# Kernel tuning notes

Measured on AMD Instinct MI355X. Metric: run time of the kernel, lower is better.

## Reference

```python
import jax, jax.numpy as jnp
import numpy as np

NUM_HEAD = 8
EPS = 1e-12  # matches torch F.normalize default eps


def setup_inputs() -> dict:
    key = jax.random.key(0)
    k1, k2, k3 = jax.random.split(key, 3)
    B, N, C = 8, 8192, 384
    x = jax.random.normal(k1, (B, N, C), dtype=jnp.float32)
    # torch Linear weights: (out_features, in_features)
    w_qkv = jax.random.normal(k2, (3 * C, C), dtype=jnp.float32) * (C ** -0.5)
    w_proj = jax.random.normal(k3, (C, C), dtype=jnp.float32) * (C ** -0.5)
    b_proj = jnp.zeros((C,), dtype=jnp.float32)
    return {"x": x, "w_qkv": w_qkv, "w_proj": w_proj, "b_proj": b_proj}


def _l2norm(t):
    # F.normalize(t, dim=-1): t / max(||t||_2, eps)
    n = jnp.sqrt(jnp.sum(t * t, axis=-1, keepdims=True))
    return t / jnp.maximum(n, EPS)


def reference(x, w_qkv, w_proj, b_proj):
    B, N, C = x.shape
    H = NUM_HEAD
    Dh = C // H
    qkv = x @ w_qkv.T  # (B, N, 3C), qkv_bias=False
    qkv = qkv.reshape(B, N, 3, H, Dh).transpose(2, 0, 3, 1, 4)  # (3, B, H, N, Dh)
    q, k, v = qkv[0], qkv[1], qkv[2]
    # transpose(-2, -1) -> (B, H, Dh, N); normalize along N (cross-covariance attn)
    q = _l2norm(jnp.swapaxes(q, -2, -1))
    k = _l2norm(jnp.swapaxes(k, -2, -1))
    v = jnp.swapaxes(v, -2, -1)  # (B, H, Dh, N)
    attn = jnp.einsum('bhdn,bhen->bhde', q, k)  # (B, H, Dh, Dh)
    attn = jax.nn.softmax(attn, axis=-1)
    out = jnp.einsum('bhde,bhen->bhdn', attn, v)  # (B, H, Dh, N)
    out = out.transpose(0, 3, 1, 2).reshape(B, N, C)  # (B, N, C)
    out = out @ w_proj.T + b_proj
    return out
```

## Files before the change

kernel.cpp:

```cpp
#include <hip/hip_runtime.h>
#include <hip/hip_bf16.h>
#include <stdint.h>


typedef __bf16 bf16_t;
typedef __attribute__((ext_vector_type(8))) __bf16 bf16x8;
typedef __attribute__((ext_vector_type(4))) __bf16 bf16x4;
typedef __attribute__((ext_vector_type(4))) float f32x4;

#define NTOK 8192
#define CDIM 384
#define WH   25165824
#define DHN  393216

#define XCHUNKS 3145728
#define TCHUNKS 3201024

__device__ __forceinline__ f32x4 mfma16(bf16x8 a, bf16x8 b, f32x4 c) {
  return __builtin_amdgcn_mfma_f32_16x16x32_bf16(a, b, c, 0, 0, 0);
}

__device__ __forceinline__ void gload16(bf16_t* lds, const bf16_t* g) {
  __builtin_amdgcn_global_load_lds(
      (const __attribute__((address_space(1))) void*)g,
      (__attribute__((address_space(3))) void*)lds, 16, 0, 0);
}

template <bool BF16>
__device__ __forceinline__ bf16x8 load8(const void* p, int idx) {
  if constexpr (BF16) {
    return *(const bf16x8*)((const bf16_t*)p + idx);
  } else {
    const float* f = (const float*)p + idx;
    f32x4 a = *(const f32x4*)f;
    f32x4 b = *(const f32x4*)(f + 4);
    bf16x8 r;
    r[0] = (bf16_t)a[0]; r[1] = (bf16_t)a[1]; r[2] = (bf16_t)a[2]; r[3] = (bf16_t)a[3];
    r[4] = (bf16_t)b[0]; r[5] = (bf16_t)b[1]; r[6] = (bf16_t)b[2]; r[7] = (bf16_t)b[3];
    return r;
  }
}

__global__ void k_probe(const uint32_t* __restrict__ X, int* __restrict__ flag) {
  __shared__ int cnt;
  if (threadIdx.x == 0) cnt = 0;
  __syncthreads();
  const uint32_t w = X[threadIdx.x];
  const int e = (int)((w >> 7) & 0xFF);
  const int sane = (e >= 110 && e <= 131) ? 1 : 0;
  atomicAdd(&cnt, sane);
  __syncthreads();
  if (threadIdx.x == 0) *flag = (cnt >= 128) ? 1 : 0;
}

__global__ void k_zero(float* __restrict__ p, int n) {
  int i = blockIdx.x * 256 + threadIdx.x;
  if (i < n) p[i] = 0.f;
}

__global__ void k_cvt(const void* __restrict__ X, const void* __restrict__ Wqkv,
                      bf16_t* __restrict__ Xb, bf16_t* __restrict__ Wb,
                      const int* __restrict__ flagp) {
  const int isb = *flagp;
  const int G = gridDim.x * 256;
  for (int c = blockIdx.x * 256 + threadIdx.x; c < TCHUNKS; c += G) {
    const bool isX = c < XCHUNKS;
    const int lc = isX ? c : c - XCHUNKS;
    const void* src = isX ? X : Wqkv;
    bf16_t* dst = (isX ? Xb : Wb) + (size_t)lc * 8;
    if (isb) {
      *(bf16x8*)dst = *((const bf16x8*)src + lc);
    } else {
      const f32x4 a = *((const f32x4*)src + lc * 2);
      const f32x4 b = *((const f32x4*)src + lc * 2 + 1);
      bf16x8 r;
      r[0] = (bf16_t)a[0]; r[1] = (bf16_t)a[1]; r[2] = (bf16_t)a[2]; r[3] = (bf16_t)a[3];
      r[4] = (bf16_t)b[0]; r[5] = (bf16_t)b[1]; r[6] = (bf16_t)b[2]; r[7] = (bf16_t)b[3];
      *(bf16x8*)dst = r;
    }
  }
}

template <bool BF16, bool GL>
__device__ __forceinline__ void qkv_body(const void* __restrict__ X,
                                         const void* __restrict__ Wqkv,
                                         bf16_t* __restrict__ qkv,
                                         bf16_t* As, bf16_t* Bs) {
  const int tid = threadIdx.x;
  const int lane = tid & 63;
  const int wr = tid >> 7, wc = (tid >> 6) & 1;
  const int q4 = lane >> 4, l16 = lane & 15;
  const int rowB0 = blockIdx.x * 128;
  const int r0 = tid >> 2, kk = (tid & 3) << 3;
  const int bb = rowB0 >> 13;
  const int nB = rowB0 & 8191;

  const bf16_t* XB = (const bf16_t*)X;
  const bf16_t* WB = (const bf16_t*)Wqkv;

  for (int jt = 0; jt < 9; jt++) {
    const int rowA0 = jt * 128;
    const int which = jt / 3;
    const int jtt = jt - which * 3;
    f32x4 acc[4][4];
#pragma unroll
    for (int i = 0; i < 4; i++)
#pragma unroll
      for (int j = 0; j < 4; j++) acc[i][j] = (f32x4){0.f, 0.f, 0.f, 0.f};

    for (int k0 = 0; k0 < CDIM; k0 += 32) {
      if constexpr (GL) {
        __syncthreads();
        gload16(As + tid * 8,         WB + (rowA0 + r0) * CDIM + k0 + kk);
        gload16(As + (tid + 256) * 8, WB + (rowA0 + r0 + 64) * CDIM + k0 + kk);
        gload16(Bs + tid * 8,         XB + (rowB0 + r0) * CDIM + k0 + kk);
        gload16(Bs + (tid + 256) * 8, XB + (rowB0 + r0 + 64) * CDIM + k0 + kk);
        __syncthreads();
      } else {
        bf16x8 a0 = load8<BF16>(Wqkv, (rowA0 + r0) * CDIM + k0 + kk);
        bf16x8 a1 = load8<BF16>(Wqkv, (rowA0 + r0 + 64) * CDIM + k0 + kk);
        bf16x8 b0 = load8<BF16>(X, (rowB0 + r0) * CDIM + k0 + kk);
        bf16x8 b1 = load8<BF16>(X, (rowB0 + r0 + 64) * CDIM + k0 + kk);
        __syncthreads();
        *(bf16x8*)&As[tid * 8] = a0;
        *(bf16x8*)&As[(tid + 256) * 8] = a1;
        *(bf16x8*)&Bs[tid * 8] = b0;
        *(bf16x8*)&Bs[(tid + 256) * 8] = b1;
        __syncthreads();
      }
      bf16x8 af[4], bfr[4];
#pragma unroll
      for (int i = 0; i < 4; i++) {
        af[i]  = *(const bf16x8*)&As[(wr * 64 + i * 16 + l16) * 32 + q4 * 8];
        bfr[i] = *(const bf16x8*)&Bs[(wc * 64 + i * 16 + l16) * 32 + q4 * 8];
      }
      if (which < 2) {
#pragma unroll
        for (int i = 0; i < 4; i++)
#pragma unroll
          for (int j = 0; j < 4; j++) acc[i][j] = mfma16(bfr[j], af[i], acc[i][j]);
      } else {
#pragma unroll
        for (int i = 0; i < 4; i++)
#pragma unroll
          for (int j = 0; j < 4; j++) acc[i][j] = mfma16(af[i], bfr[j], acc[i][j]);
      }
    }

    if (which < 2) {
#pragma unroll
      for (int i = 0; i < 4; i++) {
        const int rin = jtt * 128 + wr * 64 + i * 16 + l16;
        const int h = rin / 48, dh = rin - h * 48;
        bf16_t* rowp = qkv + which * WH + (bb * 8 + h) * DHN + dh * NTOK
                       + nB + wc * 64 + q4 * 4;
#pragma unroll
        for (int j = 0; j < 4; j++) {
          bf16x4 o = {(bf16_t)acc[i][j][0], (bf16_t)acc[i][j][1],
                      (bf16_t)acc[i][j][2], (bf16_t)acc[i][j][3]};
          *(bf16x4*)(rowp + j * 16) = o;
        }
      }
    } else {
#pragma unroll
      for (int i = 0; i < 4; i++) {
        const int rin0 = jtt * 128 + wr * 64 + i * 16 + q4 * 4;
#pragma unroll
        for (int j = 0; j < 4; j++) {
          const int mg = rowB0 + wc * 64 + j * 16 + l16;
          bf16x4 o = {(bf16_t)acc[i][j][0], (bf16_t)acc[i][j][1],
                      (bf16_t)acc[i][j][2], (bf16_t)acc[i][j][3]};
          *(bf16x4*)(qkv + 2 * WH + mg * CDIM + rin0) = o;
        }
      }
    }
  }
}

__global__ __launch_bounds__(256, 2) void k_gemm_qkv(
    const bf16_t* __restrict__ Xb, const bf16_t* __restrict__ Wb,
    bf16_t* __restrict__ qkv) {
  __shared__ __align__(16) bf16_t As[128 * 32];
  __shared__ __align__(16) bf16_t Bs[128 * 32];
  qkv_body<true, true>(Xb, Wb, qkv, As, Bs);
}

__global__ __launch_bounds__(256, 2) void k_gemm_qkv_bf16(
    const void* __restrict__ X, const void* __restrict__ Wqkv,
    bf16_t* __restrict__ qkv, const int* __restrict__ flagp) {
  __shared__ __align__(16) bf16_t As[128 * 32];
  __shared__ __align__(16) bf16_t Bs[128 * 32];
  if (!*flagp) return;
  qkv_body<true, false>(X, Wqkv, qkv, As, Bs);
}

__global__ __launch_bounds__(256, 2) void k_gemm_qkv_f32(
    const void* __restrict__ X, const void* __restrict__ Wqkv,
    bf16_t* __restrict__ qkv, const int* __restrict__ flagp) {
  __shared__ __align__(16) bf16_t As[128 * 32];
  __shared__ __align__(16) bf16_t Bs[128 * 32];
  if (*flagp) return;
  qkv_body<false, false>(X, Wqkv, qkv, As, Bs);
}

__global__ __launch_bounds__(256, 2) void k_gram(
    const bf16_t* __restrict__ qkv, float* __restrict__ S_acc, float* __restrict__ ssq_acc) {
  __shared__ __align__(16) float sm[9312];
  bf16_t* Qs = (bf16_t*)sm;
  bf16_t* Ks = Qs + 6144;
  float* ssq_sm = sm + 9216;

  const int tid = threadIdx.x;
  const int wave = tid >> 6, lane = tid & 63, q4 = lane >> 4, l16 = lane & 15;
  const int s = blockIdx.x, bh = blockIdx.y;
  const bf16_t* Qg = qkv + bh * DHN;
  const bf16_t* Kg = qkv + WH + bh * DHN;

  if (tid < 96) ssq_sm[tid] = 0.f;

  f32x4 acc[3][3];
#pragma unroll
  for (int i = 0; i < 3; i++)
#pragma unroll
    for (int j = 0; j < 3; j++) acc[i][j] = (f32x4){0.f, 0.f, 0.f, 0.f};
  float qss[3] = {0.f, 0.f, 0.f}, kss[3] = {0.f, 0.f, 0.f};

  for (int t0 = 0; t0 < 8; t0++) {
    const int n0 = s * 1024 + t0 * 128;
    bf16x8 qv[3], kv[3];
#pragma unroll
    for (int jj = 0; jj < 3; jj++) {
      const int c = jj * 256 + tid;
      const int st = c / 192, rem = c - st * 192;
      const int row = rem >> 2, kk = (rem & 3) << 3;
      const int gofs = row * NTOK + n0 + st * 32 + kk;
      qv[jj] = *(const bf16x8*)(Qg + gofs);
      kv[jj] = *(const bf16x8*)(Kg + gofs);
    }
    __syncthreads();
#pragma unroll
    for (int jj = 0; jj < 3; jj++) {
      *(bf16x8*)&Qs[(jj * 256 + tid) * 8] = qv[jj];
      *(bf16x8*)&Ks[(jj * 256 + tid) * 8] = kv[jj];
    }
    __syncthreads();
    bf16x8 qf[3], kf[3];
#pragma unroll
    for (int i = 0; i < 3; i++) {
      qf[i] = *(const bf16x8*)&Qs[wave * 1536 + (i * 16 + l16) * 32 + q4 * 8];
      kf[i] = *(const bf16x8*)&Ks[wave * 1536 + (i * 16 + l16) * 32 + q4 * 8];
    }
#pragma unroll
    for (int i = 0; i < 3; i++) {
#pragma unroll
      for (int u = 0; u < 8; u++) {
        const float qv2 = (float)qf[i][u], kv2 = (float)kf[i][u];
        qss[i] += qv2 * qv2;
        kss[i] += kv2 * kv2;
      }
#pragma unroll
      for (int j = 0; j < 3; j++) acc[i][j] = mfma16(qf[i], kf[j], acc[i][j]);
    }
  }

  __syncthreads();
  float* red = sm;
#pragma unroll
  for (int i = 0; i < 3; i++)
#pragma unroll
    for (int j = 0; j < 3; j++)
#pragma unroll
      for (int r = 0; r < 4; r++)
        red[wave * 2304 + (i * 3 + j) * 256 + lane * 4 + r] = acc[i][j][r];
#pragma unroll
  for (int i = 0; i < 3; i++) {
    atomicAdd(&ssq_sm[i * 16 + l16], qss[i]);
    atomicAdd(&ssq_sm[48 + i * 16 + l16], kss[i]);
  }
  __syncthreads();
  for (int idx = tid; idx < 2304; idx += 256) {
    const float v = red[idx] + red[2304 + idx] + red[4608 + idx] + red[6912 + idx];
    const int tile = idx >> 8, ln = (idx >> 2) & 63, r = idx & 3;
    const int i = tile / 3, j = tile - i * 3;
    const int d = i * 16 + ((ln >> 4) << 2) + r;
    const int e = j * 16 + (ln & 15);
    atomicAdd(&S_acc[bh * 2304 + d * 48 + e], v);
  }
  if (tid < 96) atomicAdd(&ssq_acc[bh * 96 + tid], ssq_sm[tid]);
}

__global__ void k_softmax(const float* __restrict__ S_acc, const float* __restrict__ ssq_acc,
                          float* __restrict__ attn_f) {
  __shared__ float invk_sm[48];
  const int bh = blockIdx.x, d = threadIdx.x;
  if (d < 48) invk_sm[d] = 1.f / fmaxf(sqrtf(ssq_acc[bh * 96 + 48 + d]), 1e-12f);
  __syncthreads();
  if (d < 48) {
    const float invq = 1.f / fmaxf(sqrtf(ssq_acc[bh * 96 + d]), 1e-12f);
    float lg[48], mx = -1e30f;
#pragma unroll
    for (int e = 0; e < 48; e++) {
      lg[e] = S_acc[bh * 2304 + d * 48 + e] * invq * invk_sm[e];
      mx = fmaxf(mx, lg[e]);
    }
    float ssum = 0.f;
#pragma unroll
    for (int e = 0; e < 48; e++) { lg[e] = expf(lg[e] - mx); ssum += lg[e]; }
    const float inv = 1.f / ssum;
#pragma unroll
    for (int e = 0; e < 48; e++) attn_f[bh * 2304 + d * 48 + e] = lg[e] * inv;
  }
}

__global__ void k_weff(
    const float* __restrict__ attn_f, const void* __restrict__ Wp,
    bf16_t* __restrict__ Weff, const int* __restrict__ flagp) {
  __shared__ float a_sm[2304];
  __shared__ float w_sm[2304];
  const int isb = *flagp;
  const int bid = blockIdx.x;
  const int ct = bid & 7, h = (bid >> 3) & 7, b = bid >> 6;
  const int bh = b * 8 + h;
  const int tid = threadIdx.x;

  for (int i = tid; i < 2304; i += 256) {
    a_sm[i] = attn_f[bh * 2304 + i];
    const int r = i / 48, c = i - r * 48;
    const int gi = (ct * 48 + r) * CDIM + h * 48 + c;
    w_sm[i] = isb ? (float)((const bf16_t*)Wp)[gi] : ((const float*)Wp)[gi];
  }
  __syncthreads();

  for (int o = tid; o < 2304; o += 256) {
    const int r = o / 48, e = o - r * 48;
    float s = 0.f;
#pragma unroll 8
    for (int d = 0; d < 48; d++) s += w_sm[r * 48 + d] * a_sm[d * 48 + e];
    Weff[b * 147456 + (ct * 48 + r) * CDIM + h * 48 + e] = (bf16_t)s;
  }
}

__global__ __launch_bounds__(256, 2) void k_gemm_out(
    const bf16_t* __restrict__ Weff, const bf16_t* __restrict__ qkv,
    const void* __restrict__ bias, void* __restrict__ out, const int* __restrict__ flagp) {
  __shared__ __align__(16) bf16_t As[128 * 32];
  __shared__ __align__(16) bf16_t Bs[128 * 32];
  const int isb = *flagp;
  const int tid = threadIdx.x;
  const int lane = tid & 63;
  const int wr = tid >> 7, wc = (tid >> 6) & 1;
  const int q4 = lane >> 4, l16 = lane & 15;
  const int b = blockIdx.y;
  const int rowB0 = blockIdx.x * 128;
  const bf16_t* Aa = Weff + b * 147456;
  const bf16_t* Ba = qkv + 2 * WH + b * (NTOK * CDIM);
  const int r0 = tid >> 2, kk = (tid & 3) << 3;

  for (int ct = 0; ct < 3; ct++) {
    const int rowA0 = ct * 128;
    f32x4 acc[4][4];
#pragma unroll
    for (int i = 0; i < 4; i++)
#pragma unroll
      for (int j = 0; j < 4; j++) acc[i][j] = (f32x4){0.f, 0.f, 0.f, 0.f};

    for (int k0 = 0; k0 < CDIM; k0 += 32) {
      __syncthreads();
      gload16(As + tid * 8,         Aa + (rowA0 + r0) * CDIM + k0 + kk);
      gload16(As + (tid + 256) * 8, Aa + (rowA0 + r0 + 64) * CDIM + k0 + kk);
      gload16(Bs + tid * 8,         Ba + (rowB0 + r0) * CDIM + k0 + kk);
      gload16(Bs + (tid + 256) * 8, Ba + (rowB0 + r0 + 64) * CDIM + k0 + kk);
      __syncthreads();
      bf16x8 af[4], bfr[4];
#pragma unroll
      for (int i = 0; i < 4; i++) {
        af[i]  = *(const bf16x8*)&As[(wr * 64 + i * 16 + l16) * 32 + q4 * 8];
        bfr[i] = *(const bf16x8*)&Bs[(wc * 64 + i * 16 + l16) * 32 + q4 * 8];
      }
#pragma unroll
      for (int i = 0; i < 4; i++)
#pragma unroll
        for (int j = 0; j < 4; j++) acc[i][j] = mfma16(af[i], bfr[j], acc[i][j]);
    }

#pragma unroll
    for (int i = 0; i < 4; i++) {
      const int cg = rowA0 + wr * 64 + i * 16 + q4 * 4;
      float bv[4];
#pragma unroll
      for (int r = 0; r < 4; r++)
        bv[r] = isb ? (float)((const bf16_t*)bias)[cg + r] : ((const float*)bias)[cg + r];
#pragma unroll
      for (int j = 0; j < 4; j++) {
        const int ng = rowB0 + wc * 64 + j * 16 + l16;
        const int oi = (b * NTOK + ng) * CDIM + cg;
        if (isb) {
          bf16x4 o = {(bf16_t)(acc[i][j][0] + bv[0]), (bf16_t)(acc[i][j][1] + bv[1]),
                      (bf16_t)(acc[i][j][2] + bv[2]), (bf16_t)(acc[i][j][3] + bv[3])};
          *(bf16x4*)((bf16_t*)out + oi) = o;
        } else {
          f32x4 o = {acc[i][j][0] + bv[0], acc[i][j][1] + bv[1],
                     acc[i][j][2] + bv[2], acc[i][j][3] + bv[3]};
          *(f32x4*)((float*)out + oi) = o;
        }
      }
    }
  }
}

extern "C" void kernel_launch(void* const* d_in, const int* in_sizes, int n_in,
                              void* d_out, int out_size, void* d_ws, size_t ws_size,
                              hipStream_t stream) {
  (void)in_sizes; (void)n_in; (void)out_size;
  const void* X    = d_in[0];
  const void* Wqkv = d_in[1];
  const void* Wp   = d_in[2];
  const void* bias = d_in[3];

  char* ws = (char*)d_ws;
  bf16_t* qkv    = (bf16_t*)ws;
  float*  S_acc  = (float*)(ws + 150994944);
  float*  ssq    = (float*)(ws + 151584768);
  float*  attn_f = (float*)(ws + 151609344);
  bf16_t* Weff   = (bf16_t*)(ws + 152199168);
  int*    flag   = (int*)(ws + 154558464);
  bf16_t* Xb     = (bf16_t*)(ws + 154558720);
  bf16_t* Wb     = (bf16_t*)(ws + 204890368);

  const bool have_cvt_ws = ws_size >= 205775104ULL;

  k_probe<<<dim3(1), 256, 0, stream>>>((const uint32_t*)X, flag);
  k_zero<<<dim3(600), 256, 0, stream>>>(S_acc, 153600);
  if (have_cvt_ws) {
    k_cvt<<<dim3(2048), 256, 0, stream>>>(X, Wqkv, Xb, Wb, flag);
    k_gemm_qkv<<<dim3(512), 256, 0, stream>>>(Xb, Wb, qkv);
  } else {
    k_gemm_qkv_bf16<<<dim3(512), 256, 0, stream>>>(X, Wqkv, qkv, flag);
    k_gemm_qkv_f32<<<dim3(512), 256, 0, stream>>>(X, Wqkv, qkv, flag);
  }
  k_gram<<<dim3(8, 64), 256, 0, stream>>>(qkv, S_acc, ssq);
  k_softmax<<<dim3(64), 64, 0, stream>>>(S_acc, ssq, attn_f);
  k_weff<<<dim3(512), 256, 0, stream>>>(attn_f, Wp, Weff, flag);
  k_gemm_out<<<dim3(64, 8), 256, 0, stream>>>(Weff, qkv, bias, d_out, flag);
}
```

Baseline: 407.1 us.

## Double-buffer LDS tiles in QKV and output GEMMs to overlap loads with MFMA

Adds ping-pong LDS buffers to the direct-to-LDS QKV GEMM and the output GEMM. The next k-slice (crossing output-tile boundaries) is issued before computing on the current one, with one barrier per iteration instead of two. This is meant to hide global load latency behind MFMA work, at the cost of doubling LDS use per block, which may reduce occupancy. The legacy register-staged paths are split into a separate function and left unchanged.

```diff
diff --git a/kernel.cpp b/kernel.cpp
--- a/kernel.cpp
+++ b/kernel.cpp
@@ -81,11 +81,10 @@
   }
 }
 
-template <bool BF16, bool GL>
-__device__ __forceinline__ void qkv_body(const void* __restrict__ X,
-                                         const void* __restrict__ Wqkv,
-                                         bf16_t* __restrict__ qkv,
-                                         bf16_t* As, bf16_t* Bs) {
+__device__ __forceinline__ void qkv_body_pipe(const bf16_t* __restrict__ XB,
+                                              const bf16_t* __restrict__ WB,
+                                              bf16_t* __restrict__ qkv,
+                                              bf16_t* As, bf16_t* Bs) {
   const int tid = threadIdx.x;
   const int lane = tid & 63;
   const int wr = tid >> 7, wc = (tid >> 6) & 1;
@@ -95,11 +94,22 @@
   const int bb = rowB0 >> 13;
   const int nB = rowB0 & 8191;
 
-  const bf16_t* XB = (const bf16_t*)X;
-  const bf16_t* WB = (const bf16_t*)Wqkv;
+  auto STAGE = [&](int jts, int ks, int nxt) {
+    const int rowA0 = jts * 128;
+    const int k0 = ks * 32;
+    bf16_t* Ad = As + nxt * 4096;
+    bf16_t* Bd = Bs + nxt * 4096;
+    gload16(Ad + tid * 8,         WB + (rowA0 + r0) * CDIM + k0 + kk);
+    gload16(Ad + (tid + 256) * 8, WB + (rowA0 + r0 + 64) * CDIM + k0 + kk);
+    gload16(Bd + tid * 8,         XB + (rowB0 + r0) * CDIM + k0 + kk);
+    gload16(Bd + (tid + 256) * 8, XB + (rowB0 + r0 + 64) * CDIM + k0 + kk);
+  };
+
+  STAGE(0, 0, 0);
+  __syncthreads();
+  int cur = 0;
 
   for (int jt = 0; jt < 9; jt++) {
-    const int rowA0 = jt * 128;
     const int which = jt / 3;
     const int jtt = jt - which * 3;
     f32x4 acc[4][4];
@@ -108,31 +118,19 @@
 #pragma unroll
       for (int j = 0; j < 4; j++) acc[i][j] = (f32x4){0.f, 0.f, 0.f, 0.f};
 
-    for (int k0 = 0; k0 < CDIM; k0 += 32) {
-      if constexpr (GL) {
-        __syncthreads();
-        gload16(As + tid * 8,         WB + (rowA0 + r0) * CDIM + k0 + kk);
-        gload16(As + (tid + 256) * 8, WB + (rowA0 + r0 + 64) * CDIM + k0 + kk);
-        gload16(Bs + tid * 8,         XB + (rowB0 + r0) * CDIM + k0 + kk);
-        gload16(Bs + (tid + 256) * 8, XB + (rowB0 + r0 + 64) * CDIM + k0 + kk);
-        __syncthreads();
-      } else {
-        bf16x8 a0 = load8<BF16>(Wqkv, (rowA0 + r0) * CDIM + k0 + kk);
-        bf16x8 a1 = load8<BF16>(Wqkv, (rowA0 + r0 + 64) * CDIM + k0 + kk);
-        bf16x8 b0 = load8<BF16>(X, (rowB0 + r0) * CDIM + k0 + kk);
-        bf16x8 b1 = load8<BF16>(X, (rowB0 + r0 + 64) * CDIM + k0 + kk);
-        __syncthreads();
-        *(bf16x8*)&As[tid * 8] = a0;
-        *(bf16x8*)&As[(tid + 256) * 8] = a1;
-        *(bf16x8*)&Bs[tid * 8] = b0;
-        *(bf16x8*)&Bs[(tid + 256) * 8] = b1;
-        __syncthreads();
-      }
+    for (int k = 0; k < 12; k++) {
+      if (!(jt == 8 && k == 11)) {
+        int kn = k + 1, jn = jt;
+        if (kn == 12) { kn = 0; jn = jt + 1; }
+        STAGE(jn, kn, cur ^ 1);
+      }
+      const bf16_t* Ac = As + cur * 4096;
+      const bf16_t* Bc = Bs + cur * 4096;
       bf16x8 af[4], bfr[4];
 #pragma unroll
       for (int i = 0; i < 4; i++) {
-        af[i]  = *(const bf16x8*)&As[(wr * 64 + i * 16 + l16) * 32 + q4 * 8];
-        bfr[i] = *(const bf16x8*)&Bs[(wc * 64 + i * 16 + l16) * 32 + q4 * 8];
+        af[i]  = *(const bf16x8*)&Ac[(wr * 64 + i * 16 + l16) * 32 + q4 * 8];
+        bfr[i] = *(const bf16x8*)&Bc[(wc * 64 + i * 16 + l16) * 32 + q4 * 8];
       }
       if (which < 2) {
 #pragma unroll
@@ -145,6 +143,8 @@
 #pragma unroll
           for (int j = 0; j < 4; j++) acc[i][j] = mfma16(af[i], bfr[j], acc[i][j]);
       }
+      __syncthreads();
+      cur ^= 1;
     }
 
     if (which < 2) {
@@ -180,9 +180,93 @@
 __global__ __launch_bounds__(256, 2) void k_gemm_qkv(
     const bf16_t* __restrict__ Xb, const bf16_t* __restrict__ Wb,
     bf16_t* __restrict__ qkv) {
-  __shared__ __align__(16) bf16_t As[128 * 32];
-  __shared__ __align__(16) bf16_t Bs[128 * 32];
-  qkv_body<true, true>(Xb, Wb, qkv, As, Bs);
+  __shared__ __align__(16) bf16_t As[2 * 4096];
+  __shared__ __align__(16) bf16_t Bs[2 * 4096];
+  qkv_body_pipe(Xb, Wb, qkv, As, Bs);
+}
+
+template <bool BF16>
+__device__ __forceinline__ void qkv_body_legacy(const void* __restrict__ X,
+                                                const void* __restrict__ Wqkv,
+                                                bf16_t* __restrict__ qkv,
+                                                bf16_t* As, bf16_t* Bs) {
+  const int tid = threadIdx.x;
+  const int lane = tid & 63;
+  const int wr = tid >> 7, wc = (tid >> 6) & 1;
+  const int q4 = lane >> 4, l16 = lane & 15;
+  const int rowB0 = blockIdx.x * 128;
+  const int r0 = tid >> 2, kk = (tid & 3) << 3;
+  const int bb = rowB0 >> 13;
+  const int nB = rowB0 & 8191;
+
+  for (int jt = 0; jt < 9; jt++) {
+    const int rowA0 = jt * 128;
+    const int which = jt / 3;
+    const int jtt = jt - which * 3;
+    f32x4 acc[4][4];
+#pragma unroll
+    for (int i = 0; i < 4; i++)
+#pragma unroll
+      for (int j = 0; j < 4; j++) acc[i][j] = (f32x4){0.f, 0.f, 0.f, 0.f};
+
+    for (int k0 = 0; k0 < CDIM; k0 += 32) {
+      bf16x8 a0 = load8<BF16>(Wqkv, (rowA0 + r0) * CDIM + k0 + kk);
+      bf16x8 a1 = load8<BF16>(Wqkv, (rowA0 + r0 + 64) * CDIM + k0 + kk);
+      bf16x8 b0 = load8<BF16>(X, (rowB0 + r0) * CDIM + k0 + kk);
+      bf16x8 b1 = load8<BF16>(X, (rowB0 + r0 + 64) * CDIM + k0 + kk);
+      __syncthreads();
+      *(bf16x8*)&As[tid * 8] = a0;
+      *(bf16x8*)&As[(tid + 256) * 8] = a1;
+      *(bf16x8*)&Bs[tid * 8] = b0;
+      *(bf16x8*)&Bs[(tid + 256) * 8] = b1;
+      __syncthreads();
+      bf16x8 af[4], bfr[4];
+#pragma unroll
+      for (int i = 0; i < 4; i++) {
+        af[i]  = *(const bf16x8*)&As[(wr * 64 + i * 16 + l16) * 32 + q4 * 8];
+        bfr[i] = *(const bf16x8*)&Bs[(wc * 64 + i * 16 + l16) * 32 + q4 * 8];
+      }
+      if (which < 2) {
+#pragma unroll
+        for (int i = 0; i < 4; i++)
+#pragma unroll
+          for (int j = 0; j < 4; j++) acc[i][j] = mfma16(bfr[j], af[i], acc[i][j]);
+      } else {
+#pragma unroll
+        for (int i = 0; i < 4; i++)
+#pragma unroll
+          for (int j = 0; j < 4; j++) acc[i][j] = mfma16(af[i], bfr[j], acc[i][j]);
+      }
+    }
+
+    if (which < 2) {
+#pragma unroll
+      for (int i = 0; i < 4; i++) {
+        const int rin = jtt * 128 + wr * 64 + i * 16 + l16;
+        const int h = rin / 48, dh = rin - h * 48;
+        bf16_t* rowp = qkv + which * WH + (bb * 8 + h) * DHN + dh * NTOK
+                       + nB + wc * 64 + q4 * 4;
+#pragma unroll
+        for (int j = 0; j < 4; j++) {
+          bf16x4 o = {(bf16_t)acc[i][j][0], (bf16_t)acc[i][j][1],
+                      (bf16_t)acc[i][j][2], (bf16_t)acc[i][j][3]};
+          *(bf16x4*)(rowp + j * 16) = o;
+        }
+      }
+    } else {
+#pragma unroll
+      for (int i = 0; i < 4; i++) {
+        const int rin0 = jtt * 128 + wr * 64 + i * 16 + q4 * 4;
+#pragma unroll
+        for (int j = 0; j < 4; j++) {
+          const int mg = rowB0 + wc * 64 + j * 16 + l16;
+          bf16x4 o = {(bf16_t)acc[i][j][0], (bf16_t)acc[i][j][1],
+                      (bf16_t)acc[i][j][2], (bf16_t)acc[i][j][3]};
+          *(bf16x4*)(qkv + 2 * WH + mg * CDIM + rin0) = o;
+        }
+      }
+    }
+  }
 }
 
 __global__ __launch_bounds__(256, 2) void k_gemm_qkv_bf16(
@@ -191,7 +275,7 @@
   __shared__ __align__(16) bf16_t As[128 * 32];
   __shared__ __align__(16) bf16_t Bs[128 * 32];
   if (!*flagp) return;
-  qkv_body<true, false>(X, Wqkv, qkv, As, Bs);
+  qkv_body_legacy<true>(X, Wqkv, qkv, As, Bs);
 }
 
 __global__ __launch_bounds__(256, 2) void k_gemm_qkv_f32(
@@ -200,7 +284,7 @@
   __shared__ __align__(16) bf16_t As[128 * 32];
   __shared__ __align__(16) bf16_t Bs[128 * 32];
   if (*flagp) return;
-  qkv_body<false, false>(X, Wqkv, qkv, As, Bs);
+  qkv_body_legacy<false>(X, Wqkv, qkv, As, Bs);
 }
 
 __global__ __launch_bounds__(256, 2) void k_gram(
@@ -343,8 +427,8 @@
 __global__ __launch_bounds__(256, 2) void k_gemm_out(
     const bf16_t* __restrict__ Weff, const bf16_t* __restrict__ qkv,
     const void* __restrict__ bias, void* __restrict__ out, const int* __restrict__ flagp) {
-  __shared__ __align__(16) bf16_t As[128 * 32];
-  __shared__ __align__(16) bf16_t Bs[128 * 32];
+  __shared__ __align__(16) bf16_t As[2 * 4096];
+  __shared__ __align__(16) bf16_t Bs[2 * 4096];
   const int isb = *flagp;
   const int tid = threadIdx.x;
   const int lane = tid & 63;
@@ -356,6 +440,21 @@
   const bf16_t* Ba = qkv + 2 * WH + b * (NTOK * CDIM);
   const int r0 = tid >> 2, kk = (tid & 3) << 3;
 
+  auto STAGE = [&](int cts, int ks, int nxt) {
+    const int rowA0 = cts * 128;
+    const int k0 = ks * 32;
+    bf16_t* Ad = As + nxt * 4096;
+    bf16_t* Bd = Bs + nxt * 4096;
+    gload16(Ad + tid * 8,         Aa + (rowA0 + r0) * CDIM + k0 + kk);
+    gload16(Ad + (tid + 256) * 8, Aa + (rowA0 + r0 + 64) * CDIM + k0 + kk);
+    gload16(Bd + tid * 8,         Ba + (rowB0 + r0) * CDIM + k0 + kk);
+    gload16(Bd + (tid + 256) * 8, Ba + (rowB0 + r0 + 64) * CDIM + k0 + kk);
+  };
+
+  STAGE(0, 0, 0);
+  __syncthreads();
+  int cur = 0;
+
   for (int ct = 0; ct < 3; ct++) {
     const int rowA0 = ct * 128;
     f32x4 acc[4][4];
@@ -364,23 +463,26 @@
 #pragma unroll
       for (int j = 0; j < 4; j++) acc[i][j] = (f32x4){0.f, 0.f, 0.f, 0.f};
 
-    for (int k0 = 0; k0 < CDIM; k0 += 32) {
+    for (int k = 0; k < 12; k++) {
+      if (!(ct == 2 && k == 11)) {
+        int kn = k + 1, cn = ct;
+        if (kn == 12) { kn = 0; cn = ct + 1; }
+        STAGE(cn, kn, cur ^ 1);
+      }
+      const bf16_t* Ac = As + cur * 4096;
+      const bf16_t* Bc = Bs + cur * 4096;
+      bf16x8 af[4], bfr[4];
+#pragma unroll
+      for (int i = 0; i < 4; i++) {
+        af[i]  = *(const bf16x8*)&Ac[(wr * 64 + i * 16 + l16) * 32 + q4 * 8];
+        bfr[i] = *(const bf16x8*)&Bc[(wc * 64 + i * 16 + l16) * 32 + q4 * 8];
+      }
+#pragma unroll
+      for (int i = 0; i < 4; i++)
+#pragma unroll
+        for (int j = 0; j < 4; j++) acc[i][j] = mfma16(af[i], bfr[j], acc[i][j]);
       __syncthreads();
-      gload16(As + tid * 8,         Aa + (rowA0 + r0) * CDIM + k0 + kk);
-      gload16(As + (tid + 256) * 8, Aa + (rowA0 + r0 + 64) * CDIM + k0 + kk);
-      gload16(Bs + tid * 8,         Ba + (rowB0 + r0) * CDIM + k0 + kk);
-      gload16(Bs + (tid + 256) * 8, Ba + (rowB0 + r0 + 64) * CDIM + k0 + kk);
-      __syncthreads();
-      bf16x8 af[4], bfr[4];
-#pragma unroll
-      for (int i = 0; i < 4; i++) {
-        af[i]  = *(const bf16x8*)&As[(wr * 64 + i * 16 + l16) * 32 + q4 * 8];
-        bfr[i] = *(const bf16x8*)&Bs[(wc * 64 + i * 16 + l16) * 32 + q4 * 8];
-      }
-#pragma unroll
-      for (int i = 0; i < 4; i++)
-#pragma unroll
-        for (int j = 0; j < 4; j++) acc[i][j] = mfma16(af[i], bfr[j], acc[i][j]);
+      cur ^= 1;
     }
 
 #pragma unroll
```

Result: no change. 408.8 us (+0.4%).
